# Performance work log

Hardware: AMD Instinct MI355X
Metric: run time of the kernel (lower is better)

The kernel has to match this reference:

```python
import jax, jax.numpy as jnp
import numpy as np


def setup_inputs() -> dict:
    key = jax.random.key(0)
    k1, k2 = jax.random.split(key)
    N, M, D = 8192, 8192, 64
    x = jax.random.normal(k1, (N, D), dtype=jnp.float32)
    y = jax.random.normal(k2, (M, D), dtype=jnp.float32)
    gamma = jnp.asarray(1.0, dtype=jnp.float32)  # scalar gamma per __init__ default
    return {"x": x, "y": y, "gamma": gamma}


def reference(x, y, gamma):
    # dist2[i,j] = sum_d (x[i,d] - y[j,d])^2 = |x_i|^2 + |y_j|^2 - 2 x_i . y_j
    # Uses the GEMM trick instead of materializing the [N, M, D] broadcast diff.
    x2 = jnp.sum(x * x, axis=-1)[:, None]          # [N, 1]
    y2 = jnp.sum(y * y, axis=-1)[None, :]          # [1, M]
    xy = jnp.einsum('nd,md->nm', x, y)             # [N, M]
    dist2 = x2 + y2 - 2.0 * xy                     # [N, M]
    return jnp.exp(-gamma * dist2)
```

## Files before the change

### kernel.cpp

```cpp
#include <hip/hip_runtime.h>

typedef float f32x4 __attribute__((ext_vector_type(4)));
typedef short s16x8 __attribute__((ext_vector_type(8)));

#if __has_builtin(__builtin_amdgcn_exp2f)
#define EXP2F(x) __builtin_amdgcn_exp2f(x)
#else
#define EXP2F(x) __expf((x) * 0.6931471805599453f)
#endif

__device__ inline unsigned short bf16_rne(float v) {
    unsigned u = __float_as_uint(v);
    u += 0x7FFFu + ((u >> 16) & 1u);
    return (unsigned short)(u >> 16);
}

__global__ __launch_bounds__(256) void rbf_pack(
        const float* __restrict__ x, const float* __restrict__ y,
        const float* __restrict__ gamma_p, float* __restrict__ nrm,
        unsigned short* __restrict__ xpk, unsigned short* __restrict__ ypk,
        int N, int M) {
    const int t = threadIdx.x;
    const int r = blockIdx.x * 32 + (t >> 3);
    const int c = t & 7;
    if (r >= N + M) return;
    const int isX = r < N;
    const int rr = isX ? r : (r - N);
    const float* src = (isX ? x : y) + (size_t)rr * 64 + c * 8;
    f32x4 t0 = *(const f32x4*)src;
    f32x4 t1 = *(const f32x4*)(src + 4);

    s16x8 h, l;
    #pragma unroll
    for (int j = 0; j < 4; ++j) {
        unsigned short hb = bf16_rne(t0[j]);
        float hf = __uint_as_float((unsigned)hb << 16);
        h[j] = (short)hb; l[j] = (short)bf16_rne(t0[j] - hf);
        hb = bf16_rne(t1[j]);
        hf = __uint_as_float((unsigned)hb << 16);
        h[4+j] = (short)hb; l[4+j] = (short)bf16_rne(t1[j] - hf);
    }

    float sn = t0[0]*t0[0] + t0[1]*t0[1] + t0[2]*t0[2] + t0[3]*t0[3]
             + t1[0]*t1[0] + t1[1]*t1[1] + t1[2]*t1[2] + t1[3]*t1[3];
    sn += __shfl_xor(sn, 1);
    sn += __shfl_xor(sn, 2);
    sn += __shfl_xor(sn, 4);
    if (c == 0)
        nrm[r] = -(*gamma_p) * 1.4426950408889634f * sn;

    const int prow = rr & 127;
    const size_t pbase = (size_t)(rr >> 7) * 2048;
    const size_t uh = pbase + prow * 8 + (c ^ (prow & 7));
    unsigned short* pk = isX ? xpk : ypk;
    *(s16x8*)(pk + uh * 8) = h;
    *(s16x8*)(pk + (uh + 1024) * 8) = l;
}

#define LROW 68
__global__ __launch_bounds__(256, 2) void rbf_main(
        const unsigned short* __restrict__ xpk, const unsigned short* __restrict__ ypk,
        const float* __restrict__ gamma_p, const float* __restrict__ nrm,
        float* __restrict__ out, int N, int M, int nbm, int nbn) {
    __shared__ char smem[65536];

    int bm, bn;
    const int nwg = nbm * nbn;
    if ((nwg & 7) == 0 && (nbm & 7) == 0) {
        const int xcd = blockIdx.x & 7;
        const int lo  = blockIdx.x >> 3;
        const int bmPerX = nbm >> 3;
        bn = lo / bmPerX;
        bm = xcd * bmPerX + (lo - bn * bmPerX);
    } else {
        bm = blockIdx.x / nbn;
        bn = blockIdx.x - bm * nbn;
    }

    const int tid = threadIdx.x;
    const int lane = tid & 63;
    const int wid = tid >> 6;
    const int wr = wid >> 1, wc = wid & 1;
    const int brow = bm * 128 + wr * 64;
    const int bcol = bn * 128 + wc * 64;
    const int l15 = lane & 15;
    const int lg  = lane >> 4;

    f32x4 acc[4][4];
    #pragma unroll
    for (int i = 0; i < 4; ++i)
        #pragma unroll
        for (int j = 0; j < 4; ++j)
            #pragma unroll
            for (int e = 0; e < 4; ++e)
                acc[i][j][e] = 0.0f;

    {
        const char* srcA = (const char*)xpk + (size_t)bm * 32768;
        const char* srcB = (const char*)ypk + (size_t)bn * 32768;
        #pragma unroll
        for (int it = 0; it < 16; ++it) {
            const int isB = it >> 3;
            const int local = (it & 7) * 4096 + wid * 1024;
            const char* src = (isB ? srcB : srcA) + local + lane * 16;
            char* dst = smem + isB * 32768 + local;
#if __has_builtin(__builtin_amdgcn_global_load_lds)
            __builtin_amdgcn_global_load_lds(
                (const __attribute__((address_space(1))) void*)src,
                (__attribute__((address_space(3))) void*)dst, 16, 0, 0);
#else
            *(s16x8*)(dst + lane * 16) = *(const s16x8*)src;
#endif
        }
    }
    __syncthreads();

    s16x8 ah[4], al[4], bh[4], bl[4];
    #pragma unroll
    for (int k0 = 0; k0 < 64; k0 += 32) {
        const int kc = (k0 >> 3) + lg;
        #pragma unroll
        for (int mf = 0; mf < 4; ++mf) {
            const int arow = wr * 64 + mf * 16 + l15;
            const int off = arow * 128 + ((kc ^ (arow & 7)) << 4);
            ah[mf] = *(const s16x8*)(smem + off);
            al[mf] = *(const s16x8*)(smem + 16384 + off);
        }
        #pragma unroll
        for (int nf = 0; nf < 4; ++nf) {
            const int brw = wc * 64 + nf * 16 + l15;
            const int off = brw * 128 + ((kc ^ (brw & 7)) << 4);
            bh[nf] = *(const s16x8*)(smem + 32768 + off);
            bl[nf] = *(const s16x8*)(smem + 49152 + off);
        }
        #pragma unroll
        for (int mf = 0; mf < 4; ++mf)
            #pragma unroll
            for (int nf = 0; nf < 4; ++nf) {
                acc[mf][nf] = __builtin_amdgcn_mfma_f32_16x16x32_bf16(ah[mf], bh[nf], acc[mf][nf], 0, 0, 0);
                acc[mf][nf] = __builtin_amdgcn_mfma_f32_16x16x32_bf16(ah[mf], bl[nf], acc[mf][nf], 0, 0, 0);
                acc[mf][nf] = __builtin_amdgcn_mfma_f32_16x16x32_bf16(al[mf], bh[nf], acc[mf][nf], 0, 0, 0);
            }
    }
    __syncthreads();

    const float g = *gamma_p;
    const float two_s = 2.0f * g * 1.4426950408889634f;
    const float* nx = nrm;
    const float* ny = nrm + N;

    float yn[4];
    #pragma unroll
    for (int nf = 0; nf < 4; ++nf)
        yn[nf] = ny[bcol + nf * 16 + l15];

    float* wl = (float*)smem + wid * 16 * LROW;

    #pragma unroll
    for (int mf = 0; mf < 4; ++mf) {
        float xn[4];
        #pragma unroll
        for (int j = 0; j < 4; ++j)
            xn[j] = nx[brow + mf * 16 + lg * 4 + j];

        #pragma unroll
        for (int nf = 0; nf < 4; ++nf) {
            const int c = nf * 16 + l15;
            #pragma unroll
            for (int j = 0; j < 4; ++j) {
                const float d = fmaf(two_s, acc[mf][nf][j], xn[j] + yn[nf]);
                wl[(lg * 4 + j) * LROW + c] = EXP2F(d);
            }
        }
        #pragma unroll
        for (int t = 0; t < 4; ++t) {
            const int r = t * 4 + lg;
            f32x4 v = *(const f32x4*)&wl[r * LROW + l15 * 4];
            float* dst = out + (size_t)(brow + mf * 16 + r) * M + bcol + l15 * 4;
            *(f32x4*)dst = v;
        }
    }
}

__global__ __launch_bounds__(256, 2) void rbf_fused_nows(
        const float* __restrict__ x, const float* __restrict__ y,
        const float* __restrict__ gamma_p,
        float* __restrict__ out, int N, int M, int nbm, int nbn) {
    __shared__ char smem[65536];
    __shared__ float nrmAB[256];

    int bm, bn;
    const int nwg = nbm * nbn;
    if ((nwg & 7) == 0 && (nbm & 7) == 0) {
        const int xcd = blockIdx.x & 7;
        const int lo  = blockIdx.x >> 3;
        const int bmPerX = nbm >> 3;
        bn = lo / bmPerX;
        bm = xcd * bmPerX + (lo - bn * bmPerX);
    } else {
        bm = blockIdx.x / nbn;
        bn = blockIdx.x - bm * nbn;
    }

    const int tid = threadIdx.x;
    const int lane = tid & 63;
    const int wid = tid >> 6;
    const int wr = wid >> 1, wc = wid & 1;
    const int brow = bm * 128 + wr * 64;
    const int bcol = bn * 128 + wc * 64;
    const int l15 = lane & 15;
    const int lg  = lane >> 4;

    const float g = *gamma_p;
    const float negs = -g * 1.4426950408889634f;
    const float two_s = 2.0f * g * 1.4426950408889634f;

    f32x4 acc[4][4];
    #pragma unroll
    for (int i = 0; i < 4; ++i)
        #pragma unroll
        for (int j = 0; j < 4; ++j)
            #pragma unroll
            for (int e = 0; e < 4; ++e)
                acc[i][j][e] = 0.0f;

    {
        const float* srcx = x + (size_t)bm * 128 * 64;
        const float* srcy = y + (size_t)bn * 128 * 64;
        #pragma unroll
        for (int it = 0; it < 8; ++it) {
            const int u = it * 256 + tid;
            const int isy = it >> 2;
            const int v = u & 1023;
            const int row = v >> 3, kc = v & 7;
            const float* s = (isy ? srcy : srcx) + (size_t)row * 64 + kc * 8;
            f32x4 t0 = *(const f32x4*)s;
            f32x4 t1 = *(const f32x4*)(s + 4);
            s16x8 h, l;
            #pragma unroll
            for (int j = 0; j < 4; ++j) {
                unsigned short hb = bf16_rne(t0[j]);
                float hf = __uint_as_float((unsigned)hb << 16);
                h[j] = (short)hb; l[j] = (short)bf16_rne(t0[j] - hf);
                hb = bf16_rne(t1[j]);
                hf = __uint_as_float((unsigned)hb << 16);
                h[4+j] = (short)hb; l[4+j] = (short)bf16_rne(t1[j] - hf);
            }
            const int dst = (isy << 15) + row * 128 + ((kc ^ (row & 7)) << 4);
            *(s16x8*)(smem + dst) = h;
            *(s16x8*)(smem + dst + 16384) = l;
            float sn = t0[0]*t0[0] + t0[1]*t0[1] + t0[2]*t0[2] + t0[3]*t0[3]
                     + t1[0]*t1[0] + t1[1]*t1[1] + t1[2]*t1[2] + t1[3]*t1[3];
            sn += __shfl_xor(sn, 1);
            sn += __shfl_xor(sn, 2);
            sn += __shfl_xor(sn, 4);
            if (kc == 0) nrmAB[(isy << 7) + row] = negs * sn;
        }
    }
    __syncthreads();

    s16x8 ah[4], al[4], bh[4], bl[4];
    #pragma unroll
    for (int k0 = 0; k0 < 64; k0 += 32) {
        const int kc = (k0 >> 3) + lg;
        #pragma unroll
        for (int mf = 0; mf < 4; ++mf) {
            const int arow = wr * 64 + mf * 16 + l15;
            const int off = arow * 128 + ((kc ^ (arow & 7)) << 4);
            ah[mf] = *(const s16x8*)(smem + off);
            al[mf] = *(const s16x8*)(smem + 16384 + off);
        }
        #pragma unroll
        for (int nf = 0; nf < 4; ++nf) {
            const int brw = wc * 64 + nf * 16 + l15;
            const int off = brw * 128 + ((kc ^ (brw & 7)) << 4);
            bh[nf] = *(const s16x8*)(smem + 32768 + off);
            bl[nf] = *(const s16x8*)(smem + 49152 + off);
        }
        #pragma unroll
        for (int mf = 0; mf < 4; ++mf)
            #pragma unroll
            for (int nf = 0; nf < 4; ++nf) {
                acc[mf][nf] = __builtin_amdgcn_mfma_f32_16x16x32_bf16(ah[mf], bh[nf], acc[mf][nf], 0, 0, 0);
                acc[mf][nf] = __builtin_amdgcn_mfma_f32_16x16x32_bf16(ah[mf], bl[nf], acc[mf][nf], 0, 0, 0);
                acc[mf][nf] = __builtin_amdgcn_mfma_f32_16x16x32_bf16(al[mf], bh[nf], acc[mf][nf], 0, 0, 0);
            }
    }
    __syncthreads();

    float yn[4];
    #pragma unroll
    for (int nf = 0; nf < 4; ++nf)
        yn[nf] = nrmAB[128 + wc * 64 + nf * 16 + l15];

    float* wl = (float*)smem + wid * 16 * LROW;
    #pragma unroll
    for (int mf = 0; mf < 4; ++mf) {
        float xn[4];
        #pragma unroll
        for (int j = 0; j < 4; ++j)
            xn[j] = nrmAB[wr * 64 + mf * 16 + lg * 4 + j];
        #pragma unroll
        for (int nf = 0; nf < 4; ++nf) {
            const int c = nf * 16 + l15;
            #pragma unroll
            for (int j = 0; j < 4; ++j) {
                const float d = fmaf(two_s, acc[mf][nf][j], xn[j] + yn[nf]);
                wl[(lg * 4 + j) * LROW + c] = EXP2F(d);
            }
        }
        #pragma unroll
        for (int t = 0; t < 4; ++t) {
            const int r = t * 4 + lg;
            f32x4 v = *(const f32x4*)&wl[r * LROW + l15 * 4];
            float* dst = out + (size_t)(brow + mf * 16 + r) * M + bcol + l15 * 4;
            *(f32x4*)dst = v;
        }
    }
}

extern "C" void kernel_launch(void* const* d_in, const int* in_sizes, int n_in,
                              void* d_out, int out_size, void* d_ws, size_t ws_size,
                              hipStream_t stream) {
    const float* x = (const float*)d_in[0];
    const float* y = (const float*)d_in[1];
    const float* gamma_p = (const float*)d_in[2];
    float* out = (float*)d_out;

    const int D = 64;
    const int N = in_sizes[0] / D;
    const int M = in_sizes[1] / D;
    const int nbm = N / 128, nbn = M / 128;

    char* wsb = (char*)d_ws;
    float* nrm = (float*)wsb;
    size_t off = ((size_t)(N + M) * 4 + 15) & ~(size_t)15;
    unsigned short* xpk = (unsigned short*)(wsb + off); off += (size_t)N * 128 * 2;
    unsigned short* ypk = (unsigned short*)(wsb + off); off += (size_t)M * 128 * 2;

    if (ws_size >= off) {
        const int rows = N + M;
        rbf_pack<<<(rows + 31) / 32, 256, 0, stream>>>(x, y, gamma_p, nrm, xpk, ypk, N, M);
        rbf_main<<<nbm * nbn, 256, 0, stream>>>(xpk, ypk, gamma_p, nrm, out, N, M, nbm, nbn);
    } else {
        rbf_fused_nows<<<nbm * nbn, 256, 0, stream>>>(x, y, gamma_p, out, N, M, nbm, nbn);
    }
}
```

Measured before the change: 59.31 us.

## Add multi-tile kernel keeping A in registers and double-buffering B tiles

Adds a kernel where each workgroup handles a strip of eight column tiles for one row block. The A panel and x norms stay in registers across the strip, and the next B tile is prefetched into LDS (global_load_lds) while the current tile is computed and written out. This removes the repeated A loads and the per-workgroup launch and prologue cost, and overlaps B loading with the exp/store epilogue. The trade-off is fewer workgroups (512), higher register pressure from keeping A in registers, and a hand-written vmcnt wait that relies on an exact count of outstanding loads.

```diff
diff --git a/kernel.cpp b/kernel.cpp
--- a/kernel.cpp
+++ b/kernel.cpp
@@ -58,6 +58,157 @@
 }
 
 #define LROW 68
+#define NT 8
+
+__global__ __launch_bounds__(256, 2) void rbf_persist(
+        const unsigned short* __restrict__ xpk, const unsigned short* __restrict__ ypk,
+        const float* __restrict__ gamma_p, const float* __restrict__ nrm,
+        float* __restrict__ out, int N, int M, int nbm, int nbn) {
+    __shared__ char smem[65536];
+
+    const int xcd = blockIdx.x & 7;
+    const int idx = blockIdx.x >> 3;
+    const int bmPerX = nbm >> 3;
+    const int bm = xcd * bmPerX + (idx % bmPerX);
+    const int strip = idx / bmPerX;
+    const int bn0 = strip * NT;
+
+    const int tid = threadIdx.x;
+    const int lane = tid & 63;
+    const int wid = tid >> 6;
+    const int wr = wid >> 1, wc = wid & 1;
+    const int brow = bm * 128 + wr * 64;
+    const int l15 = lane & 15;
+    const int lg  = lane >> 4;
+
+    const float g = *gamma_p;
+    const float two_s = 2.0f * g * 1.4426950408889634f;
+    const float* ny = nrm + N;
+
+    s16x8 ah[2][4], al[2][4];
+    {
+        const unsigned short* apan = xpk + (size_t)bm * 16384;
+        #pragma unroll
+        for (int ks = 0; ks < 2; ++ks) {
+            const int kc = ks * 4 + lg;
+            #pragma unroll
+            for (int mf = 0; mf < 4; ++mf) {
+                const int arow = wr * 64 + mf * 16 + l15;
+                const int u = arow * 8 + (kc ^ (arow & 7));
+                ah[ks][mf] = *(const s16x8*)(apan + (size_t)u * 8);
+                al[ks][mf] = *(const s16x8*)(apan + (size_t)(u + 1024) * 8);
+            }
+        }
+    }
+    float xn[4][4];
+    #pragma unroll
+    for (int mf = 0; mf < 4; ++mf)
+        #pragma unroll
+        for (int j = 0; j < 4; ++j)
+            xn[mf][j] = nrm[brow + mf * 16 + lg * 4 + j];
+
+    {
+        const char* src = (const char*)ypk + (size_t)bn0 * 32768;
+        #pragma unroll
+        for (int it = 0; it < 8; ++it) {
+            const int local = it * 4096 + wid * 1024;
+            __builtin_amdgcn_global_load_lds(
+                (const __attribute__((address_space(1))) void*)(src + local + lane * 16),
+                (__attribute__((address_space(3))) void*)(smem + local), 16, 0, 0);
+        }
+    }
+    __builtin_amdgcn_sched_barrier(0);
+    asm volatile("s_waitcnt vmcnt(0)" ::: "memory");
+    __builtin_amdgcn_sched_barrier(0);
+    __builtin_amdgcn_s_barrier();
+    __builtin_amdgcn_sched_barrier(0);
+
+    for (int i = 0; i < NT; ++i) {
+        const int cur = i & 1;
+        const int bn = bn0 + i;
+        const int bcol = bn * 128 + wc * 64;
+
+        float yn[4];
+        #pragma unroll
+        for (int nf = 0; nf < 4; ++nf)
+            yn[nf] = ny[bcol + nf * 16 + l15];
+
+        if (i + 1 < NT) {
+            const char* src = (const char*)ypk + (size_t)(bn + 1) * 32768;
+            char* dstb = smem + (cur ^ 1) * 32768;
+            #pragma unroll
+            for (int it = 0; it < 8; ++it) {
+                const int local = it * 4096 + wid * 1024;
+                __builtin_amdgcn_global_load_lds(
+                    (const __attribute__((address_space(1))) void*)(src + local + lane * 16),
+                    (__attribute__((address_space(3))) void*)(dstb + local), 16, 0, 0);
+            }
+        }
+
+        const char* bufb = smem + cur * 32768;
+        f32x4 acc[4][4];
+        #pragma unroll
+        for (int a = 0; a < 4; ++a)
+            #pragma unroll
+            for (int b = 0; b < 4; ++b)
+                #pragma unroll
+                for (int e = 0; e < 4; ++e)
+                    acc[a][b][e] = 0.0f;
+
+        #pragma unroll
+        for (int ks = 0; ks < 2; ++ks) {
+            const int kc = ks * 4 + lg;
+            s16x8 bh[4], bl[4];
+            #pragma unroll
+            for (int nf = 0; nf < 4; ++nf) {
+                const int brw = wc * 64 + nf * 16 + l15;
+                const int off = brw * 128 + ((kc ^ (brw & 7)) << 4);
+                bh[nf] = *(const s16x8*)(bufb + off);
+                bl[nf] = *(const s16x8*)(bufb + 16384 + off);
+            }
+            #pragma unroll
+            for (int mf = 0; mf < 4; ++mf)
+                #pragma unroll
+                for (int nf = 0; nf < 4; ++nf) {
+                    acc[mf][nf] = __builtin_amdgcn_mfma_f32_16x16x32_bf16(ah[ks][mf], bh[nf], acc[mf][nf], 0, 0, 0);
+                    acc[mf][nf] = __builtin_amdgcn_mfma_f32_16x16x32_bf16(ah[ks][mf], bl[nf], acc[mf][nf], 0, 0, 0);
+                    acc[mf][nf] = __builtin_amdgcn_mfma_f32_16x16x32_bf16(al[ks][mf], bh[nf], acc[mf][nf], 0, 0, 0);
+                }
+        }
+
+        __builtin_amdgcn_sched_barrier(0);
+        __builtin_amdgcn_s_barrier();
+        __builtin_amdgcn_sched_barrier(0);
+
+        float* wl = (float*)(smem + cur * 32768) + wid * 16 * LROW;
+        #pragma unroll
+        for (int mf = 0; mf < 4; ++mf) {
+            #pragma unroll
+            for (int nf = 0; nf < 4; ++nf) {
+                const int c = nf * 16 + l15;
+                #pragma unroll
+                for (int j = 0; j < 4; ++j) {
+                    const float d = fmaf(two_s, acc[mf][nf][j], xn[mf][j] + yn[nf]);
+                    wl[(lg * 4 + j) * LROW + c] = EXP2F(d);
+                }
+            }
+            #pragma unroll
+            for (int t = 0; t < 4; ++t) {
+                const int r = t * 4 + lg;
+                f32x4 v = *(const f32x4*)&wl[r * LROW + l15 * 4];
+                float* dst = out + (size_t)(brow + mf * 16 + r) * M + bcol + l15 * 4;
+                *(f32x4*)dst = v;
+            }
+        }
+
+        __builtin_amdgcn_sched_barrier(0);
+        asm volatile("s_waitcnt vmcnt(16)" ::: "memory");
+        __builtin_amdgcn_sched_barrier(0);
+        __builtin_amdgcn_s_barrier();
+        __builtin_amdgcn_sched_barrier(0);
+    }
+}
+
 __global__ __launch_bounds__(256, 2) void rbf_main(
         const unsigned short* __restrict__ xpk, const unsigned short* __restrict__ ypk,
         const float* __restrict__ gamma_p, const float* __restrict__ nrm,
@@ -104,13 +255,9 @@
             const int local = (it & 7) * 4096 + wid * 1024;
             const char* src = (isB ? srcB : srcA) + local + lane * 16;
             char* dst = smem + isB * 32768 + local;
-#if __has_builtin(__builtin_amdgcn_global_load_lds)
             __builtin_amdgcn_global_load_lds(
                 (const __attribute__((address_space(1))) void*)src,
                 (__attribute__((address_space(3))) void*)dst, 16, 0, 0);
-#else
-            *(s16x8*)(dst + lane * 16) = *(const s16x8*)src;
-#endif
         }
     }
     __syncthreads();
@@ -146,23 +293,19 @@
 
     const float g = *gamma_p;
     const float two_s = 2.0f * g * 1.4426950408889634f;
-    const float* nx = nrm;
-    const float* ny = nrm + N;
 
     float yn[4];
     #pragma unroll
     for (int nf = 0; nf < 4; ++nf)
-        yn[nf] = ny[bcol + nf * 16 + l15];
+        yn[nf] = (nrm + N)[bcol + nf * 16 + l15];
 
     float* wl = (float*)smem + wid * 16 * LROW;
-
     #pragma unroll
     for (int mf = 0; mf < 4; ++mf) {
         float xn[4];
         #pragma unroll
         for (int j = 0; j < 4; ++j)
-            xn[j] = nx[brow + mf * 16 + lg * 4 + j];
-
+            xn[j] = nrm[brow + mf * 16 + lg * 4 + j];
         #pragma unroll
         for (int nf = 0; nf < 4; ++nf) {
             const int c = nf * 16 + l15;
@@ -341,7 +484,12 @@
     if (ws_size >= off) {
         const int rows = N + M;
         rbf_pack<<<(rows + 31) / 32, 256, 0, stream>>>(x, y, gamma_p, nrm, xpk, ypk, N, M);
-        rbf_main<<<nbm * nbn, 256, 0, stream>>>(xpk, ypk, gamma_p, nrm, out, N, M, nbm, nbn);
+        if ((nbm % 8) == 0 && (nbn % NT) == 0) {
+            const int grid = nbm * (nbn / NT);
+            rbf_persist<<<grid, 256, 0, stream>>>(xpk, ypk, gamma_p, nrm, out, N, M, nbm, nbn);
+        } else {
+            rbf_main<<<nbm * nbn, 256, 0, stream>>>(xpk, ypk, gamma_p, nrm, out, N, M, nbm, nbn);
+        }
     } else {
         rbf_fused_nows<<<nbm * nbn, 256, 0, stream>>>(x, y, gamma_p, out, N, M, nbm, nbn);
     }
```

After: 52.23 us. 1.14x faster.
